# Kernel optimization log

Hardware: AMD Instinct MI355X
Metric: run time of the kernel (lower is better)

The kernel has to match this reference:

```python
import jax, jax.numpy as jnp
import numpy as np

V, D, H, B, S, T, N_EXTRA = 32000, 256, 512, 16, 400, 100, 50


def _lstm_cell(x, h, c, Wih, Whh, b):
    g = x @ Wih.T + h @ Whh.T + b
    i, f, gg, o = jnp.split(g, 4, axis=-1)
    c = jax.nn.sigmoid(f) * c + jax.nn.sigmoid(i) * jnp.tanh(gg)
    h = jax.nn.sigmoid(o) * jnp.tanh(c)
    return h, c


def _run_lstm(xs, m, Wih, Whh, b):
    # xs: [S,B,D], m: [S,B,1] validity mask (packed-sequence semantics)
    Bz, Hh = xs.shape[1], Whh.shape[1]
    init = (jnp.zeros((Bz, Hh), xs.dtype), jnp.zeros((Bz, Hh), xs.dtype))
    def step(carry, inp):
        h, c = carry
        x, mm = inp
        hn, cn = _lstm_cell(x, h, c, Wih, Whh, b)
        h = jnp.where(mm, hn, h)
        c = jnp.where(mm, cn, c)
        return (h, c), jnp.where(mm, hn, 0.0)
    (h, c), ys = jax.lax.scan(step, init, (xs, m))
    return ys, h, c


def setup_inputs():
    key = jax.random.key(0)
    ks = jax.random.split(key, 20)
    def gn(k, shape, scale=0.05):
        return jax.random.normal(k, shape, dtype=jnp.float32) * scale
    inp = {}
    inp["source"] = jax.random.randint(ks[0], (B, S), 0, V)
    inp["source_extended"] = jax.random.randint(ks[1], (B, S), 0, V + N_EXTRA)
    inp["source_length"] = jax.random.randint(ks[2], (B,), S // 2, S + 1)
    inp["target"] = jax.random.randint(ks[3], (B, T), 0, V)
    inp["emb"] = gn(ks[4], (V, D), 0.1)
    inp["enc_Wih_f"] = gn(ks[5], (4 * H, D))
    inp["enc_Whh_f"] = gn(ks[6], (4 * H, H))
    inp["enc_b_f"] = jnp.zeros((4 * H,), jnp.float32)
    inp["enc_Wih_b"] = gn(ks[7], (4 * H, D))
    inp["enc_Whh_b"] = gn(ks[8], (4 * H, H))
    inp["enc_b_b"] = jnp.zeros((4 * H,), jnp.float32)
    inp["Wproj"] = gn(ks[9], (H, 2 * H))
    inp["bproj"] = jnp.zeros((H,), jnp.float32)
    inp["W2h"] = gn(ks[10], (H, 2 * H))
    inp["b2h"] = jnp.zeros((H,), jnp.float32)
    inp["W2c"] = gn(ks[11], (H, 2 * H))
    inp["b2c"] = jnp.zeros((H,), jnp.float32)
    inp["Wo1"] = gn(ks[12], (H, 2 * H))
    inp["bo1"] = jnp.zeros((H,), jnp.float32)
    inp["Wo2"] = gn(ks[13], (D, H))
    inp["dec_Wih"] = gn(ks[14], (4 * H, 2 * D))
    inp["dec_Whh"] = gn(ks[15], (4 * H, H))
    inp["dec_b"] = jnp.zeros((4 * H,), jnp.float32)
    inp["Wpgen"] = gn(ks[16], (1, 2 * H + 2 * D))
    inp["bpgen"] = jnp.zeros((1,), jnp.float32)
    return inp


def reference(source, source_extended, source_length, target, emb,
              enc_Wih_f, enc_Whh_f, enc_b_f, enc_Wih_b, enc_Whh_b, enc_b_b,
              Wproj, bproj, W2h, b2h, W2c, b2c, Wo1, bo1, Wo2,
              dec_Wih, dec_Whh, dec_b, Wpgen, bpgen):
    mask = jnp.arange(S)[None, :] < source_length[:, None]  # [B,S]
    w_s = emb[source]                                        # [B,S,D]
    xs = jnp.swapaxes(w_s, 0, 1)                             # [S,B,D]
    m = jnp.swapaxes(mask, 0, 1)[:, :, None]                 # [S,B,1]
    # bidirectional LSTM encoder
    ys_f, h_f, c_f = _run_lstm(xs, m, enc_Wih_f, enc_Whh_f, enc_b_f)
    ys_b, h_b, c_b = _run_lstm(xs[::-1], m[::-1], enc_Wih_b, enc_Whh_b, enc_b_b)
    ys_b = ys_b[::-1]
    enc_outs = jnp.swapaxes(jnp.concatenate([ys_f, ys_b], -1), 0, 1)  # [B,S,2H]
    enc_outs = enc_outs @ Wproj.T + bproj                             # [B,S,H]
    dec_h = jnp.concatenate([h_f, h_b], -1) @ W2h.T + b2h             # [B,H]
    dec_c = jnp.concatenate([c_f, c_b], -1) @ W2c.T + b2c             # [B,H]
    lens = source_length[:, None].astype(enc_outs.dtype)
    seq_mean = (enc_outs * mask[..., None]).sum(1) / lens             # [B,H]
    def out_proj(x):
        return jnp.tanh(x @ Wo1.T + bo1) @ Wo2.T
    dec_out0 = out_proj(jnp.concatenate([dec_h, seq_mean], -1))       # [B,D]
    neg = jnp.finfo(enc_outs.dtype).min
    extra = jnp.zeros((B, N_EXTRA), enc_outs.dtype)
    rows = jnp.arange(B)[:, None]
    w_t = jnp.swapaxes(emb[target], 0, 1)                             # [T,B,D]
    def step(carry, x_t):
        dec_out, h, c = carry
        x = jnp.concatenate([x_t, dec_out], -1)                       # [B,2D]
        h, c = _lstm_cell(x, h, c, dec_Wih, dec_Whh, dec_b)
        scores = jnp.einsum('bh,bsh->bs', h, enc_outs)
        attn = jax.nn.softmax(jnp.where(mask, scores, neg), axis=-1)  # point_dist
        context = jnp.einsum('bs,bsh->bh', attn, enc_outs)
        p_gen = jax.nn.sigmoid(jnp.concatenate([context, h, x], -1) @ Wpgen.T + bpgen)  # [B,1]
        dec_out = out_proj(jnp.concatenate([h, context], -1))         # [B,D]
        logit = dec_out @ emb.T                                       # [B,V]
        vocab_dist = jnp.concatenate([p_gen * jax.nn.softmax(logit, axis=-1), extra], -1)
        final = vocab_dist.at[rows, source_extended].add((1.0 - p_gen) * attn) + 1e-20
        return (dec_out, h, c), jnp.log(final)
    _, logits = jax.lax.scan(step, (dec_out0, dec_h, dec_c), w_t)
    return logits  # [T,B,V+N_EXTRA]
```

## Files before the change

### kernel.cpp

```cpp
#include <hip/hip_runtime.h>

#define V_SZ 32000
#define D_SZ 256
#define H_SZ 512
#define B_SZ 16
#define S_SZ 400
#define T_SZ 100
#define G4   2048
#define VX   32050
#define LINE 32
#define SENTU 0xFFFFFFFFu

typedef unsigned short ushort_t;
typedef __attribute__((ext_vector_type(8))) __bf16 bf16x8;
typedef __attribute__((ext_vector_type(8))) unsigned short ushort8_t;
typedef __attribute__((ext_vector_type(4))) float f32x4;
typedef __attribute__((ext_vector_type(4))) unsigned u32x4;

__device__ __forceinline__ ushort_t f2bf(float x) {
  union { float f; unsigned u; } v; v.f = x;
  unsigned r = v.u + 0x7fffu + ((v.u >> 16) & 1u);
  return (ushort_t)(r >> 16);
}
__device__ __forceinline__ float bf2f(ushort_t x) {
  union { unsigned u; float f; } v; v.u = ((unsigned)x) << 16; return v.f;
}
__device__ __forceinline__ float bfu2f(unsigned x) {
  union { unsigned u; float f; } v; v.u = x << 16; return v.f;
}
__device__ __forceinline__ float sigf(float x) { return 1.0f / (1.0f + __expf(-x)); }
__device__ __forceinline__ float tanh_f(float x) {
  float e = __expf(2.0f * x);
  return 1.0f - 2.0f / (e + 1.0f);
}
__device__ __forceinline__ float dot4(f32x4 a, f32x4 b) {
  return a.x * b.x + a.y * b.y + a.z * b.z + a.w * b.w;
}
__device__ __forceinline__ void stg(float* p, float v) {
  __hip_atomic_store(p, v, __ATOMIC_RELAXED, __HIP_MEMORY_SCOPE_AGENT);
}
__device__ __forceinline__ void stg_u32(unsigned* p, unsigned v) {
  __hip_atomic_store(p, v, __ATOMIC_RELAXED, __HIP_MEMORY_SCOPE_AGENT);
}
__device__ __forceinline__ unsigned pollu(const unsigned* p) {
  return __hip_atomic_load(p, __ATOMIC_RELAXED, __HIP_MEMORY_SCOPE_AGENT);
}
__device__ __forceinline__ unsigned okq(u32x4 c) {
  return (unsigned)((c.x != SENTU) & (c.y != SENTU) & (c.z != SENTU) & (c.w != SENTU));
}
__device__ __forceinline__ u32x4 ld1_ic(const unsigned* p) {
  u32x4 v;
  asm volatile("global_load_dwordx4 %0, %1, off sc0 sc1\n\ts_waitcnt vmcnt(0)"
               : "=&v"(v) : "v"(p) : "memory");
  return v;
}

__device__ __forceinline__ void slot_barrier(unsigned* slots, int myslot, int nslots,
                                             unsigned pc) {
  asm volatile("s_waitcnt vmcnt(0)" ::: "memory");
  __syncthreads();
  if (threadIdx.x == 0)
    __hip_atomic_store(&slots[myslot * LINE], pc, __ATOMIC_RELAXED, __HIP_MEMORY_SCOPE_AGENT);
  if (threadIdx.x < 64) {
    const int i0 = threadIdx.x, i1 = threadIdx.x + 64, i2 = threadIdx.x + 128;
    for (;;) {
      unsigned v0 = pc, v1 = pc, v2 = pc;
      if (i0 < nslots) v0 = pollu(&slots[i0 * LINE]);
      if (i1 < nslots) v1 = pollu(&slots[i1 * LINE]);
      if (i2 < nslots) v2 = pollu(&slots[i2 * LINE]);
      if (__all((v0 >= pc) & (v1 >= pc) & (v2 >= pc))) break;
      __builtin_amdgcn_s_sleep(1);
    }
  }
  __syncthreads();
}

__global__ __launch_bounds__(256) void cvt_kernel(const float* in, ushort_t* outp, int n) {
  int i = blockIdx.x * 256 + threadIdx.x;
  int stride = gridDim.x * 256;
  for (; i < n; i += stride) outp[i] = f2bf(in[i]);
}

__global__ __launch_bounds__(256) void pack_whh_kernel(const float* whh_f, const float* whh_b,
                                                       ushort_t* outp) {
  int gid = blockIdx.x * 256 + threadIdx.x;
  int col = gid & 511;
  int p_g = gid >> 9;
  int dir = p_g >> 11, p = p_g & 2047;
  int ub = p >> 6, g = (p >> 4) & 3, u = p & 15;
  const float* src = dir ? whh_b : whh_f;
  outp[gid] = f2bf(src[(size_t)(g * 512 + ub * 16 + u) * 512 + col]);
}

__global__ __launch_bounds__(256) void gxT_kernel(const float* gx, float* gxT) {
  int t = blockIdx.y;
  int r = blockIdx.x * 256 + threadIdx.x;
  float v[16];
#pragma unroll
  for (int b = 0; b < 16; ++b) v[b] = gx[((size_t)t * 16 + b) * G4 + r];
  f32x4* dst = (f32x4*)(gxT + ((size_t)t * G4 + r) * 16);
#pragma unroll
  for (int q = 0; q < 4; ++q) {
    f32x4 w = {v[q * 4], v[q * 4 + 1], v[q * 4 + 2], v[q * 4 + 3]};
    dst[q] = w;
  }
}

__global__ __launch_bounds__(256) void gather_src_kernel(const ushort_t* emb_bf, const int* source,
                                                         ushort_t* xs_bf) {
  int gid = blockIdx.x * 256 + threadIdx.x;
  int r = gid >> 5, e = gid & 31;
  int s = r >> 4, b = r & 15;
  int tok = source[b * S_SZ + s];
  ((ushort8_t*)xs_bf)[gid] = ((const ushort8_t*)emb_bf)[(size_t)tok * 32 + e];
}

__device__ __forceinline__ void mfma_16x64(const ushort_t* A, const ushort_t* B_, int K,
                                           int m0, int n0, f32x4 acc[4]) {
  const int lane = threadIdx.x & 63;
  const int lr = lane & 15, kh = lane >> 4;
  const ushort_t* ap = A + (size_t)(m0 + lr) * K + kh * 8;
  const ushort_t* bp = B_ + (size_t)(n0 + lr) * K + kh * 8;
  for (int k0 = 0; k0 < K; k0 += 32) {
    bf16x8 av = *(const bf16x8*)(ap + k0);
#pragma unroll
    for (int s = 0; s < 4; ++s) {
      bf16x8 bv = *(const bf16x8*)(bp + (size_t)s * 16 * K + k0);
      acc[s] = __builtin_amdgcn_mfma_f32_16x16x32_bf16(av, bv, acc[s], 0, 0, 0);
    }
  }
}

__global__ __launch_bounds__(256) void gemm_abt_bias(const ushort_t* A, const ushort_t* Bm,
                                                     const float* bias, float* out, int K) {
  int wave = threadIdx.x >> 6;
  int m0 = blockIdx.y * 16;
  int n0 = blockIdx.x * 256 + wave * 64;
  f32x4 acc[4] = {};
  mfma_16x64(A, Bm, K, m0, n0, acc);
  int lane = threadIdx.x & 63, lr = lane & 15, kh = lane >> 4;
#pragma unroll
  for (int s = 0; s < 4; ++s) {
    int n = n0 + s * 16 + lr;
    float bv = bias[n];
#pragma unroll
    for (int i = 0; i < 4; ++i) {
      int m = m0 + kh * 4 + i;
      out[(size_t)m * G4 + n] = acc[s][i] + bv;
    }
  }
}

__global__ __launch_bounds__(256) void gemm_encout(const ushort_t* ys_cat, const ushort_t* wproj_bf,
                                                   const float* bproj, float* enc_outs) {
  int wave = threadIdx.x >> 6;
  int m0 = blockIdx.y * 16;
  int n0 = blockIdx.x * 256 + wave * 64;
  f32x4 acc[4] = {};
  mfma_16x64(ys_cat, wproj_bf, 2 * H_SZ, m0, n0, acc);
  int lane = threadIdx.x & 63, lr = lane & 15, kh = lane >> 4;
#pragma unroll
  for (int s = 0; s < 4; ++s) {
    int n = n0 + s * 16 + lr;
    float bv = bproj[n];
#pragma unroll
    for (int i = 0; i < 4; ++i) {
      int m = m0 + kh * 4 + i;
      int b = m & 15, si = m >> 4;
      enc_outs[((size_t)b * S_SZ + si) * H_SZ + n] = acc[s][i] + bv;
    }
  }
}

__global__ __launch_bounds__(256) void enc_kernel(
    const float* gx_f, const float* gx_b, const ushort_t* whh_pk, const int* src_len,
    unsigned* hbf_f, unsigned* hbf_b, unsigned* ys_cat_u32, float* h_final, float* c_final,
    unsigned* ctrs,
    const int* target, const ushort_t* emb_bf, ushort_t* xt_bf, const float* wo1,
    ushort_t* wo1_bf, const float* dwih, ushort_t* wihd_bf, const float* wo2,
    ushort_t* wo2t_bf, const float* wproj, ushort_t* wproj_bf, const float* wpgen, float* wfp,
    float* wfused, const float* dwhh, ushort_t* wdec_pk, ushort_t* e2_bf) {
  __shared__ float gates_s[4 * 16 * 17];
  __shared__ float xr_s[256];
  const int blk = blockIdx.x, tid = threadIdx.x;

  if (blk >= 64) {
    const int pid = blk - 64;
    const int gtid = pid * 256 + tid;
    const int GSTR = 192 * 256;
    for (int i = gtid; i < 512 * 1024; i += GSTR) wo1_bf[i] = f2bf(wo1[i]);
    for (int i = gtid; i < 2048 * 256; i += GSTR) {
      int r = i >> 8, d = i & 255;
      wihd_bf[i] = f2bf(dwih[(size_t)r * 512 + d]);
    }
    for (int i = gtid; i < 512 * 256; i += GSTR) {
      int h2 = i >> 8, d2 = i & 255;
      wo2t_bf[i] = f2bf(wo2[(size_t)d2 * 512 + h2]);
    }
    for (int i = gtid; i < 512 * 1024; i += GSTR) wproj_bf[i] = f2bf(wproj[i]);
    for (int i = gtid; i < 51200; i += GSTR) {
      int r = i >> 5, e = i & 31;
      int tt = r >> 4, bb = r & 15;
      int tok = target[bb * T_SZ + tt];
      ((ushort8_t*)xt_bf)[i] = ((const ushort8_t*)emb_bf)[(size_t)tok * 32 + e];
    }
    for (int h2 = gtid; h2 < 512; h2 += GSTR) {
      float a = 0;
      for (int d = 0; d < 256; ++d) a += wpgen[1280 + d] * wo2[(size_t)d * 512 + h2];
      wfp[h2] = a;
    }
    for (int r = pid; r < 2048; r += 192) {
      xr_s[tid] = dwih[(size_t)r * 512 + 256 + tid];
      __syncthreads();
      float a0 = 0, a1 = 0;
      for (int d = 0; d < 256; ++d) {
        float x = xr_s[d];
        a0 += x * wo2[(size_t)d * 512 + tid];
        a1 += x * wo2[(size_t)d * 512 + tid + 256];
      }
      wfused[(size_t)r * 512 + tid] = a0;
      wfused[(size_t)r * 512 + tid + 256] = a1;
      __syncthreads();
    }
    slot_barrier(ctrs + 2048, pid, 192, 1u);
    for (int i = gtid; i < 2048 * 1024; i += GSTR) {
      int col = i & 1023, p = i >> 10;
      int ub2 = p >> 4, g2 = (p >> 2) & 3, u2 = p & 3;
      int row = g2 * 512 + ub2 * 4 + u2;
      float v = (col < 512) ? dwhh[(size_t)row * 512 + col]
                            : wfused[(size_t)row * 512 + (col - 512)];
      wdec_pk[i] = f2bf(v);
    }
    for (int q = pid; q < 4000; q += 192) {
      int mt = q >> 1, xt2 = q & 1;
      int wave = tid >> 6;
      int m0 = mt * 16, n0 = xt2 * 256 + wave * 64;
      f32x4 acc[4] = {};
      mfma_16x64(emb_bf, wo2t_bf, 256, m0, n0, acc);
      int lane2 = tid & 63, lr2 = lane2 & 15, kh2 = lane2 >> 4;
#pragma unroll
      for (int s = 0; s < 4; ++s) {
        int n = n0 + s * 16 + lr2;
#pragma unroll
        for (int i = 0; i < 4; ++i) {
          int m = m0 + kh2 * 4 + i;
          e2_bf[(size_t)m * 512 + n] = f2bf(acc[s][i]);
        }
      }
    }
    return;
  }

  const int dir = blk >> 5, ub = blk & 31, j0 = ub * 16;
  const int g = tid >> 6, lane = tid & 63, lr = lane & 15, kh = lane >> 4;
  const float* gx = dir ? gx_b : gx_f;
  unsigned* hb = dir ? hbf_b : hbf_f;
  unsigned* slots = ctrs + dir * 1024;
  const ushort_t* wrow =
      whh_pk + (size_t)(((dir * 32 + ub) * 4 + g) * 16 + lr) * 512 + kh * 8;
  const int bc = tid >> 4, uc = tid & 15;
  const int len_b = src_len[bc];
  float c_reg = 0.0f, h_reg = 0.0f;

  int maxlen;
  {
    int v = src_len[lane & 15];
    v = max(v, __shfl_xor(v, 1));
    v = max(v, __shfl_xor(v, 2));
    v = max(v, __shfl_xor(v, 4));
    v = max(v, __shfl_xor(v, 8));
    maxlen = v;
  }
  for (int i = tid; i < (S_SZ - maxlen) * 128; i += 256) {
    int s = maxlen + (i >> 7);
    int r = i & 127;
    int bb = r >> 3, k = r & 7;
    ys_cat_u32[(size_t)(s * 16 + bb) * 512 + dir * 256 + (j0 >> 1) + k] = 0u;
  }

  float gxa[4];
  {
    const int s0 = dir ? (maxlen - 1) : 0;
    const float* g0 = gx + (size_t)s0 * (16 * 2048) + g * 512 + j0 + lr;
#pragma unroll
    for (int i = 0; i < 4; ++i) gxa[i] = g0[(size_t)(kh * 4 + i) * 2048];
  }

  for (int t = 0; t < maxlen; ++t) {
    const int s_pos = dir ? (maxlen - 1 - t) : t;
    float gxn[4] = {0.f, 0.f, 0.f, 0.f};
    if (t + 1 < maxlen) {
      const int sn = dir ? (maxlen - 2 - t) : (t + 1);
      const float* gn = gx + (size_t)sn * (16 * 2048) + g * 512 + j0 + lr;
#pragma unroll
      for (int i = 0; i < 4; ++i) gxn[i] = gn[(size_t)(kh * 4 + i) * 2048];
    }
    f32x4 acc = {0.f, 0.f, 0.f, 0.f};
    const ushort_t* ap = (const ushort_t*)(hb + (size_t)t * 4096) + lr * 512 + kh * 8;
#pragma unroll
    for (int k0 = 0; k0 < 512; k0 += 32)
      acc = __builtin_amdgcn_mfma_f32_16x16x32_bf16(*(const bf16x8*)(ap + k0),
                                                    *(const bf16x8*)(wrow + k0), acc, 0, 0, 0);
#pragma unroll
    for (int i = 0; i < 4; ++i)
      gates_s[(g * 16 + lr) * 17 + kh * 4 + i] = acc[i] + gxa[i];
    __syncthreads();
    float gi = gates_s[uc * 17 + bc];
    float gf = gates_s[(16 + uc) * 17 + bc];
    float gg = gates_s[(32 + uc) * 17 + bc];
    float go = gates_s[(48 + uc) * 17 + bc];
    bool msk = s_pos < len_b;
    float cn = sigf(gf) * c_reg + sigf(gi) * tanh_f(gg);
    float hn = sigf(go) * tanh_f(cn);
    float hout = msk ? hn : h_reg;
    if (msk) c_reg = cn;
    h_reg = hout;
    unsigned hbits = (unsigned)f2bf(hout);
    unsigned hpart = __shfl_xor(hbits, 1);
    unsigned ybits = msk ? (unsigned)f2bf(hn) : 0u;
    unsigned ypart = __shfl_xor(ybits, 1);
    if ((uc & 1) == 0) {
      stg_u32(&hb[(size_t)(t + 1) * 4096 + bc * 256 + ((j0 + uc) >> 1)], hbits | (hpart << 16));
      ys_cat_u32[(size_t)(s_pos * 16 + bc) * 512 + dir * 256 + ((j0 + uc) >> 1)] =
          ybits | (ypart << 16);
    }
    if (t == maxlen - 1) {
      h_final[dir * 8192 + bc * 512 + j0 + uc] = hout;
      c_final[dir * 8192 + bc * 512 + j0 + uc] = c_reg;
    }
    if (t + 1 < maxlen) slot_barrier(slots, ub, 32, (unsigned)(t + 1));
#pragma unroll
    for (int i = 0; i < 4; ++i) gxa[i] = gxn[i];
  }
}

__global__ __launch_bounds__(256) void seqmean_kernel(const float* enc_outs, const int* src_len,
                                                      float* seq_mean) {
  int b = blockIdx.x >> 1;
  int j = (blockIdx.x & 1) * 256 + threadIdx.x;
  int L = src_len[b];
  float a = 0;
  for (int s = 0; s < L; ++s) a += enc_outs[((size_t)b * S_SZ + s) * H_SZ + j];
  seq_mean[b * 512 + j] = a / (float)L;
}

__global__ __launch_bounds__(256) void init_state_kernel(const float* h_final, const float* c_final,
                                                         const float* w2h, const float* b2h,
                                                         const float* w2c, const float* b2c,
                                                         unsigned* h_u32, float* c_init) {
  int gid = blockIdx.x * 256 + threadIdx.x;
  int half = gid >> 13;
  int idx = gid & 8191;
  int b = idx >> 9, j = idx & 511;
  const float* src = half ? c_final : h_final;
  const float* w = (half ? w2c : w2h) + (size_t)j * 1024;
  float acc = (half ? b2c : b2h)[j];
  const f32x4* s0 = (const f32x4*)(src + b * 512);
  const f32x4* s1 = (const f32x4*)(src + 8192 + b * 512);
  const f32x4* w0 = (const f32x4*)w;
  const f32x4* w1 = w0 + 128;
  float a = 0;
  for (int k = 0; k < 128; ++k) a += dot4(s0[k], w0[k]);
  for (int k = 0; k < 128; ++k) a += dot4(s1[k], w1[k]);
  acc += a;
  if (half) {
    c_init[idx] = acc;
  } else {
    unsigned bits = (unsigned)f2bf(acc);
    unsigned pb2 = __shfl_xor(bits, 1);
    if ((j & 1) == 0) h_u32[b * 256 + (j >> 1)] = bits | (pb2 << 16);
  }
}

__global__ __launch_bounds__(256) void tmp0_kernel(const unsigned* h0_u32, const float* seq_mean,
                                                   const float* wo1, const float* bo1,
                                                   unsigned* tmp_u32) {
  int gid = blockIdx.x * 256 + threadIdx.x;
  int b = gid >> 9, j = gid & 511;
  const f32x4* x1 = (const f32x4*)(seq_mean + b * 512);
  const f32x4* w0 = (const f32x4*)(wo1 + (size_t)j * 1024);
  const f32x4* w1 = w0 + 128;
  float a = bo1[j];
  float p = 0;
  const ushort_t* h0 = (const ushort_t*)(h0_u32) + b * 512;
  for (int k = 0; k < 128; ++k) {
    f32x4 hv = {bf2f(h0[k * 4]), bf2f(h0[k * 4 + 1]), bf2f(h0[k * 4 + 2]), bf2f(h0[k * 4 + 3])};
    p += dot4(hv, w0[k]);
  }
  for (int k = 0; k < 128; ++k) p += dot4(x1[k], w1[k]);
  float tv = tanh_f(a + p);
  unsigned bits = (unsigned)f2bf(tv);
  unsigned pb2 = __shfl_xor(bits, 1);
  if ((j & 1) == 0) tmp_u32[b * 256 + (j >> 1)] = bits | (pb2 << 16);
}

__global__ __launch_bounds__(256) void dec_kernel(
    const ushort_t* xt_bf, const int* src_len, const ushort_t* wdec_pk,
    const float* wpgen, const float* bpgen, const float* wfp, const ushort_t* wo1_bf,
    const float* bo1, const float* enc_outs, const float* gxT, unsigned* h_u32,
    const float* c_init, unsigned* tmp_u32, float* ctx_part, float* z_part, float* zinv,
    float* pgen_o, float* pexp, unsigned* ctrs, const ushort_t* e2_bf, float* out) {
  __shared__ ushort_t ec_s[50 * 512];
  __shared__ float part_s[4 * 16 * 17];
  __shared__ f32x4 smem4[272];
  __shared__ float red_s[8];
  __shared__ float p_s[64];
  float* sm = (float*)smem4;
  unsigned* gslots = ctrs + 8192;

  const int blk = blockIdx.x, tid = threadIdx.x;

  if (blk >= 128) {
    const int sp = blk - 128;
    unsigned* tags = ctrs + 16384;
    if (sp == 0) {
      for (int t = 0; t < T_SZ; ++t) {
        if (tid < 64) {
          const unsigned* hp = tmp_u32 + (size_t)(t + 1) * 4096 + tid * 64;
          for (;;) {
            unsigned ok = 1;
#pragma unroll
            for (int k = 0; k < 16; ++k) ok &= okq(ld1_ic(hp + k * 4));
            if (__all((int)ok)) break;
            __builtin_amdgcn_s_sleep(8);
          }
          if (tid == 0) stg_u32(&tags[t * 32], 1u);
        }
        __syncthreads();
      }
    } else if (sp <= 125) {
      const ushort_t* tmp_bf2 = (const ushort_t*)(tmp_u32 + 4096);
      const int wave = tid >> 6;
      const int n0 = (sp - 1) * 256 + wave * 64;
      const int lane2 = tid & 63, lr2 = lane2 & 15, kh2 = lane2 >> 4;
      for (int t = 0; t < T_SZ; ++t) {
        if (tid < 64) {
          while (pollu(&tags[t * 32]) == 0u) __builtin_amdgcn_s_sleep(4);
        }
        __syncthreads();
        f32x4 acc[4] = {};
        mfma_16x64(tmp_bf2, e2_bf, 512, t * 16, n0, acc);
#pragma unroll
        for (int s = 0; s < 4; ++s) {
          int n = n0 + s * 16 + lr2;
#pragma unroll
          for (int i = 0; i < 4; ++i) {
            int m = t * 16 + kh2 * 4 + i;
            out[(size_t)m * VX + n] = acc[s][i];
          }
        }
      }
    }
    return;
  }

  const int w = tid >> 6, lane = tid & 63, lr = lane & 15, kh = lane >> 4;
  const int j0 = blk * 4;
  const ushort_t* wrow = wdec_pk + (size_t)(blk * 16 + lr) * 1024 + w * 256 + kh * 8;
  const int b_c = (tid >> 2) & 15, u_c = tid & 3;
  float c_reg = (tid < 64) ? c_init[b_c * 512 + j0 + u_c] : 0.0f;
  const int b_pb = blk >> 3, ch = blk & 7, s0c = ch * 50;
  const int len_pb = src_len[b_pb];
  const int nc = ch;
  unsigned* grslots = ctrs + 12288 + b_pb * 256;
  unsigned gpc = 0;

  {
    const f32x4* ebase = (const f32x4*)(enc_outs + ((size_t)b_pb * S_SZ + s0c) * H_SZ);
    unsigned* dst = (unsigned*)ec_s;
    for (int i = tid; i < 6400; i += 256) {
      f32x4 v = ebase[i];
      dst[2 * i] = (unsigned)f2bf(v.x) | ((unsigned)f2bf(v.y) << 16);
      dst[2 * i + 1] = (unsigned)f2bf(v.z) | ((unsigned)f2bf(v.w) << 16);
    }
  }

  float gxa[4] = {0.f, 0.f, 0.f, 0.f};
  if (tid < 64) {
#pragma unroll
    for (int g2 = 0; g2 < 4; ++g2)
      gxa[g2] = gxT[((size_t)(g2 * 512 + j0 + u_c)) * 16 + b_c];
  }

  for (int t = 0; t < T_SZ; ++t) {
    {
      f32x4 acc = {0.f, 0.f, 0.f, 0.f};
      const unsigned* asrc = (w < 2) ? (h_u32 + (size_t)t * 4096) : (tmp_u32 + (size_t)t * 4096);
      const ushort_t* ap = (const ushort_t*)asrc + lr * 512 + (w & 1) * 256 + kh * 8;
#pragma unroll
      for (int k0 = 0; k0 < 256; k0 += 32)
        acc = __builtin_amdgcn_mfma_f32_16x16x32_bf16(*(const bf16x8*)(ap + k0),
                                                      *(const bf16x8*)(wrow + k0), acc, 0, 0, 0);
#pragma unroll
      for (int i = 0; i < 4; ++i) part_s[(w * 16 + lr) * 17 + kh * 4 + i] = acc[i];
      __syncthreads();
      if (tid < 64) {
        float gt[4];
#pragma unroll
        for (int g2 = 0; g2 < 4; ++g2) {
          int p = g2 * 4 + u_c;
          float a = gxa[g2];
#pragma unroll
          for (int w2 = 0; w2 < 4; ++w2) a += part_s[(w2 * 16 + p) * 17 + b_c];
          gt[g2] = a;
        }
        float cn = sigf(gt[1]) * c_reg + sigf(gt[0]) * tanh_f(gt[2]);
        c_reg = cn;
        float hn = sigf(gt[3]) * tanh_f(cn);
        unsigned bits = (unsigned)f2bf(hn);
        unsigned pb2 = __shfl_xor(bits, 1);
        if ((u_c & 1) == 0)
          stg_u32(&h_u32[(size_t)(t + 1) * 4096 + b_c * 256 + ((j0 + u_c) >> 1)],
                  bits | (pb2 << 16));
      }
    }
    slot_barrier(gslots, blk, 128, ++gpc);
    {
      if (tid < 64 && t + 1 < T_SZ) {
#pragma unroll
        for (int g2 = 0; g2 < 4; ++g2)
          gxa[g2] = gxT[((size_t)(t + 1) * G4 + g2 * 512 + j0 + u_c) * 16 + b_c];
      }
      if (tid < 128) {
        unsigned v0 = h_u32[(size_t)(t + 1) * 4096 + b_pb * 256 + tid * 2];
        unsigned v1 = h_u32[(size_t)(t + 1) * 4096 + b_pb * 256 + tid * 2 + 1];
        f32x4 hv = {bfu2f(v0 & 0xffffu), bfu2f(v0 >> 16), bfu2f(v1 & 0xffffu), bfu2f(v1 >> 16)};
        ((f32x4*)sm)[tid] = hv;
      }
      __syncthreads();
      int st = tid >> 2, kq = tid & 3;
      if (st < 50) {
        const ushort8_t* er = (const ushort8_t*)(ec_s + st * 512) + kq * 16;
        const f32x4* hr = (const f32x4*)sm + kq * 32;
        float sc = 0;
#pragma unroll 4
        for (int k = 0; k < 16; ++k) {
          ushort8_t w8 = er[k];
          f32x4 w0 = {bf2f(w8[0]), bf2f(w8[1]), bf2f(w8[2]), bf2f(w8[3])};
          f32x4 w1 = {bf2f(w8[4]), bf2f(w8[5]), bf2f(w8[6]), bf2f(w8[7])};
          sc += dot4(hr[2 * k], w0) + dot4(hr[2 * k + 1], w1);
        }
        sc += __shfl_xor(sc, 1);
        sc += __shfl_xor(sc, 2);
        if (kq == 0) {
          int s_abs = s0c + st;
          float p = (s_abs < len_pb) ? __expf(sc) : 0.0f;
          p_s[st] = p;
          pexp[((size_t)t * 16 + b_pb) * S_SZ + s_abs] = p;
        }
      }
      __syncthreads();
      if (tid == 0) {
        float z = 0;
        for (int s = 0; s < 50; ++s) z += p_s[s];
        stg(&z_part[((size_t)t * 16 + b_pb) * 8 + ch], z);
      }
      float a0 = 0, a1 = 0;
      for (int s = 0; s < 50; ++s) {
        float p = p_s[s];
        a0 += p * bf2f(ec_s[s * 512 + tid]);
        a1 += p * bf2f(ec_s[s * 512 + tid + 256]);
      }
      float* cp = ctx_part + (((size_t)t * 16 + b_pb) * 8 + ch) * 512;
      stg(&cp[tid], a0);
      stg(&cp[tid + 256], a1);
    }
    slot_barrier(grslots, ch, 8, (unsigned)(t + 1));
    {
      float* h_s = sm;
      float* ctx_s = sm + 512;
      const float* zp = z_part + ((size_t)t * 16 + b_pb) * 8;
      float z = 0;
#pragma unroll
      for (int c2 = 0; c2 < 8; ++c2) z += zp[c2];
      float inv = 1.0f / z;
      const float* cpb = ctx_part + ((size_t)t * 16 + b_pb) * 8 * 512;
      float c0 = 0, c1 = 0;
#pragma unroll
      for (int c2 = 0; c2 < 8; ++c2) {
        c0 += cpb[c2 * 512 + tid];
        c1 += cpb[c2 * 512 + tid + 256];
      }
      ctx_s[tid] = c0 * inv;
      ctx_s[tid + 256] = c1 * inv;
      __syncthreads();
      const ushort_t* tmpp = (const ushort_t*)(tmp_u32 + (size_t)t * 4096) + b_pb * 512;
      float tp0 = bf2f(tmpp[tid]);
      float tp1 = bf2f(tmpp[tid + 256]);
      float xe = bf2f(xt_bf[((size_t)t * 16 + b_pb) * 256 + tid]);
      float pg = wpgen[tid] * ctx_s[tid] + wpgen[tid + 256] * ctx_s[tid + 256] +
                 wpgen[512 + tid] * h_s[tid] + wpgen[512 + tid + 256] * h_s[tid + 256] +
                 wpgen[1024 + tid] * xe + wfp[tid] * tp0 + wfp[tid + 256] * tp1;
#pragma unroll
      for (int o = 32; o; o >>= 1) pg += __shfl_xor(pg, o);
      if (lane == 0) red_s[w] = pg;
      __syncthreads();
      if (nc == 0 && tid == 0) {
        pgen_o[t * 16 + b_pb] = sigf(red_s[0] + red_s[1] + red_s[2] + red_s[3] + bpgen[0]);
        zinv[t * 16 + b_pb] = inv;
      }
      int nidx = tid >> 2, kq = tid & 3;
      int n = nc * 64 + nidx;
      const ushort8_t* wrp = (const ushort8_t*)(wo1_bf + (size_t)n * 1024) + kq * 32;
      const f32x4* xr2 =
          (kq < 2) ? ((const f32x4*)h_s + kq * 64) : ((const f32x4*)ctx_s + (kq - 2) * 64);
      float a = 0;
#pragma unroll 4
      for (int k = 0; k < 32; ++k) {
        ushort8_t w8 = wrp[k];
        f32x4 w0 = {bf2f(w8[0]), bf2f(w8[1]), bf2f(w8[2]), bf2f(w8[3])};
        f32x4 w1 = {bf2f(w8[4]), bf2f(w8[5]), bf2f(w8[6]), bf2f(w8[7])};
        a += dot4(xr2[2 * k], w0) + dot4(xr2[2 * k + 1], w1);
      }
      a += __shfl_xor(a, 1);
      a += __shfl_xor(a, 2);
      float tv = tanh_f(a + bo1[n]);
      unsigned bits = (unsigned)f2bf(tv);
      unsigned pbits = __shfl_xor(bits, 4);
      if (kq == 0 && (nidx & 1) == 0)
        stg_u32(&tmp_u32[(size_t)(t + 1) * 4096 + b_pb * 256 + ((nc * 64 + nidx) >> 1)],
                bits | (pbits << 16));
    }
    if (t + 1 < T_SZ) slot_barrier(gslots, blk, 128, ++gpc);
  }
}

__global__ __launch_bounds__(1024) void finalize_kernel(float* out, const float* pexp,
                                                        const float* zinv, const float* pgen_i,
                                                        const int* src_ext) {
  __shared__ float scat[VX];
  __shared__ float red[64];
  const int row = blockIdx.x;
  const int b = row & 15;
  const int tid = threadIdx.x;
  for (int i = tid; i < VX; i += 1024) scat[i] = 0.0f;
  __syncthreads();
  const float pg = pgen_i[row];
  const float inv = zinv[row];
  if (tid < S_SZ) {
    float v = (1.0f - pg) * pexp[(size_t)row * S_SZ + tid] * inv;
    int col = src_ext[b * S_SZ + tid];
    atomicAdd(&scat[col], v);
  }
  float* orow = out + (size_t)row * VX;
  float l[32];
  float mx = -3.4e38f;
#pragma unroll
  for (int i2 = 0; i2 < 32; ++i2) {
    int col = tid + (i2 << 10);
    l[i2] = (col < V_SZ) ? orow[col] : -3.4e38f;
    mx = fmaxf(mx, l[i2]);
  }
#pragma unroll
  for (int o = 32; o; o >>= 1) mx = fmaxf(mx, __shfl_xor(mx, o));
  if ((tid & 63) == 0) red[16 + (tid >> 6)] = mx;
  __syncthreads();
  if (tid == 0) {
    float m2 = red[16];
    for (int w = 1; w < 16; ++w) m2 = fmaxf(m2, red[16 + w]);
    red[0] = m2;
  }
  __syncthreads();
  const float gmx = red[0];
  float se = 0.0f;
#pragma unroll
  for (int i2 = 0; i2 < 32; ++i2) {
    int col = tid + (i2 << 10);
    if (col < V_SZ) {
      l[i2] = __expf(l[i2] - gmx);
      se += l[i2];
    }
  }
#pragma unroll
  for (int o = 32; o; o >>= 1) se += __shfl_xor(se, o);
  if ((tid & 63) == 0) red[32 + (tid >> 6)] = se;
  __syncthreads();
  if (tid == 0) {
    float s2 = 0;
    for (int w = 0; w < 16; ++w) s2 += red[32 + w];
    red[1] = s2;
  }
  __syncthreads();
  const float scale = pg / red[1];
#pragma unroll
  for (int i2 = 0; i2 < 32; ++i2) {
    int col = tid + (i2 << 10);
    if (col < VX) {
      float base = (col < V_SZ) ? l[i2] * scale : 0.0f;
      orow[col] = __logf(base + scat[col] + 1e-20f);
    }
  }
}

extern "C" void kernel_launch(void* const* d_in, const int* in_sizes, int n_in, void* d_out,
                              int out_size, void* d_ws, size_t ws_size, hipStream_t stream) {
  (void)in_sizes; (void)n_in; (void)out_size; (void)ws_size;
  const int* source = (const int*)d_in[0];
  const int* source_ext = (const int*)d_in[1];
  const int* source_len = (const int*)d_in[2];
  const int* target = (const int*)d_in[3];
  const float* emb = (const float*)d_in[4];
  const float* wih_f = (const float*)d_in[5];
  const float* whh_f = (const float*)d_in[6];
  const float* b_f = (const float*)d_in[7];
  const float* wih_b = (const float*)d_in[8];
  const float* whh_b = (const float*)d_in[9];
  const float* b_b = (const float*)d_in[10];
  const float* wproj = (const float*)d_in[11];
  const float* bproj = (const float*)d_in[12];
  const float* w2h = (const float*)d_in[13];
  const float* b2h = (const float*)d_in[14];
  const float* w2c = (const float*)d_in[15];
  const float* b2c = (const float*)d_in[16];
  const float* wo1 = (const float*)d_in[17];
  const float* bo1 = (const float*)d_in[18];
  const float* wo2 = (const float*)d_in[19];
  const float* dwih = (const float*)d_in[20];
  const float* dwhh = (const float*)d_in[21];
  const float* dbias = (const float*)d_in[22];
  const float* wpgen = (const float*)d_in[23];
  const float* bpgen = (const float*)d_in[24];
  float* out = (float*)d_out;

  size_t off = 0;
  char* wsb = (char*)d_ws;
  auto alloc = [&](size_t bytes) -> void* {
    void* p = wsb + off;
    off += (bytes + 255) & ~(size_t)255;
    return p;
  };
  unsigned* ctrs = (unsigned*)alloc(80 * 1024);
  ushort_t* emb_bf = (ushort_t*)alloc((size_t)V_SZ * D_SZ * 2);
  ushort_t* wihf_bf = (ushort_t*)alloc((size_t)G4 * D_SZ * 2);
  ushort_t* wihb_bf = (ushort_t*)alloc((size_t)G4 * D_SZ * 2);
  ushort_t* wihd_bf = (ushort_t*)alloc((size_t)G4 * D_SZ * 2);
  ushort_t* wproj_bf = (ushort_t*)alloc((size_t)H_SZ * 2 * H_SZ * 2);
  ushort_t* wo2t_bf = (ushort_t*)alloc((size_t)H_SZ * D_SZ * 2);
  ushort_t* wo1_bf = (ushort_t*)alloc((size_t)H_SZ * 1024 * 2);
  float* wfused = (float*)alloc((size_t)G4 * H_SZ * 4);
  float* wfp = (float*)alloc(512 * 4);
  ushort_t* whh_pk = (ushort_t*)alloc((size_t)2 * G4 * H_SZ * 2);
  ushort_t* wdec_pk = (ushort_t*)alloc((size_t)G4 * 1024 * 2);
  ushort_t* xs_bf = (ushort_t*)alloc((size_t)S_SZ * B_SZ * D_SZ * 2);
  ushort_t* xt_bf = (ushort_t*)alloc((size_t)T_SZ * B_SZ * D_SZ * 2);
  ushort_t* e2_bf = (ushort_t*)alloc((size_t)V_SZ * H_SZ * 2);
  float* gx_f = (float*)alloc((size_t)S_SZ * B_SZ * G4 * 4);
  float* gx_b = (float*)alloc((size_t)S_SZ * B_SZ * G4 * 4);
  unsigned* hbf_f = (unsigned*)alloc((size_t)(S_SZ + 1) * 4096 * 4);
  unsigned* hbf_b = (unsigned*)alloc((size_t)(S_SZ + 1) * 4096 * 4);
  unsigned* ys_cat_u32 = (unsigned*)alloc((size_t)S_SZ * B_SZ * 512 * 4);
  float* h_final = (float*)alloc((size_t)2 * B_SZ * H_SZ * 4);
  float* c_final = (float*)alloc((size_t)2 * B_SZ * H_SZ * 4);
  float* enc_outs = (float*)alloc((size_t)B_SZ * S_SZ * H_SZ * 4);
  float* seq_mean = (float*)alloc((size_t)B_SZ * H_SZ * 4);
  unsigned* h_u32 = (unsigned*)alloc((size_t)(T_SZ + 1) * 4096 * 4);
  float* c_init = (float*)alloc((size_t)B_SZ * H_SZ * 4);
  unsigned* tmp_u32 = (unsigned*)alloc((size_t)(T_SZ + 1) * 4096 * 4);
  float* z_part = (float*)alloc((size_t)T_SZ * B_SZ * 8 * 4);
  float* zinv = (float*)alloc((size_t)T_SZ * B_SZ * 4);
  float* pgen_b = (float*)alloc((size_t)T_SZ * B_SZ * 4);
  float* pexp = (float*)alloc((size_t)T_SZ * B_SZ * S_SZ * 4);
  float* gx_dec = gx_b;
  float* ctx_part = gx_b + (size_t)3276800;
  float* gxT = gx_b + (size_t)9830400;

  hipMemsetAsync(ctrs, 0, 80 * 1024, stream);
  hipMemsetAsync(tmp_u32, 0xFF, (size_t)(T_SZ + 1) * 4096 * 4, stream);
  hipMemsetAsync(hbf_f, 0, 4096 * 4, stream);
  hipMemsetAsync(hbf_b, 0, 4096 * 4, stream);

  cvt_kernel<<<2048, 256, 0, stream>>>(emb, emb_bf, V_SZ * D_SZ);
  cvt_kernel<<<2048, 256, 0, stream>>>(wih_f, wihf_bf, G4 * D_SZ);
  cvt_kernel<<<2048, 256, 0, stream>>>(wih_b, wihb_bf, G4 * D_SZ);
  pack_whh_kernel<<<8192, 256, 0, stream>>>(whh_f, whh_b, whh_pk);
  gather_src_kernel<<<800, 256, 0, stream>>>(emb_bf, source, xs_bf);
  gemm_abt_bias<<<dim3(8, 400), 256, 0, stream>>>(xs_bf, wihf_bf, b_f, gx_f, 256);
  gemm_abt_bias<<<dim3(8, 400), 256, 0, stream>>>(xs_bf, wihb_bf, b_b, gx_b, 256);
  enc_kernel<<<256, 256, 0, stream>>>(gx_f, gx_b, whh_pk, source_len, hbf_f, hbf_b, ys_cat_u32,
                                      h_final, c_final, ctrs, target, emb_bf, xt_bf, wo1, wo1_bf,
                                      dwih, wihd_bf, wo2, wo2t_bf, wproj, wproj_bf, wpgen, wfp,
                                      wfused, dwhh, wdec_pk, e2_bf);
  gemm_encout<<<dim3(2, 400), 256, 0, stream>>>((const ushort_t*)ys_cat_u32, wproj_bf, bproj,
                                                enc_outs);
  seqmean_kernel<<<32, 256, 0, stream>>>(enc_outs, source_len, seq_mean);
  init_state_kernel<<<64, 256, 0, stream>>>(h_final, c_final, w2h, b2h, w2c, b2c, h_u32, c_init);
  tmp0_kernel<<<32, 256, 0, stream>>>(h_u32, seq_mean, wo1, bo1, tmp_u32);
  gemm_abt_bias<<<dim3(8, 100), 256, 0, stream>>>(xt_bf, wihd_bf, dbias, gx_dec, 256);
  gxT_kernel<<<dim3(8, 100), 256, 0, stream>>>(gx_dec, gxT);
  dec_kernel<<<256, 256, 0, stream>>>(xt_bf, source_len, wdec_pk, wpgen, bpgen, wfp, wo1_bf, bo1,
                                      enc_outs, gxT, h_u32, c_init, tmp_u32, ctx_part, z_part,
                                      zinv, pgen_b, pexp, ctrs, e2_bf, out);
  finalize_kernel<<<1600, 1024, 0, stream>>>(out, pexp, zinv, pgen_b, source_ext);
}
```

Baseline: 4.317 ms.

## Merge prologue conversions, batch gate GEMMs, fold decoder input GEMM into encoder helpers

The separate conversion, packing and gather kernels are merged into a single prologue kernel. The two encoder input-gate GEMMs become one launch via a z-dimension. The decoder input-projection GEMM and its transpose now run inside the encoder kernel's idle helper blocks, writing directly in the transposed gxT layout. The aim is to cut launch count and move decoder prep off the critical path. In exchange it adds work to the helper blocks, which must finish before the encoder kernel exits, and it relies on xt_bf and wihd_bf being written earlier in the same helper block.

After: 4.281 ms. About the same (-0.8%).

```diff
diff --git a/kernel.cpp b/kernel.cpp
--- a/kernel.cpp
+++ b/kernel.cpp
@@ -75,44 +75,31 @@
   __syncthreads();
 }
 
-__global__ __launch_bounds__(256) void cvt_kernel(const float* in, ushort_t* outp, int n) {
-  int i = blockIdx.x * 256 + threadIdx.x;
-  int stride = gridDim.x * 256;
-  for (; i < n; i += stride) outp[i] = f2bf(in[i]);
-}
-
-__global__ __launch_bounds__(256) void pack_whh_kernel(const float* whh_f, const float* whh_b,
-                                                       ushort_t* outp) {
-  int gid = blockIdx.x * 256 + threadIdx.x;
-  int col = gid & 511;
-  int p_g = gid >> 9;
-  int dir = p_g >> 11, p = p_g & 2047;
-  int ub = p >> 6, g = (p >> 4) & 3, u = p & 15;
-  const float* src = dir ? whh_b : whh_f;
-  outp[gid] = f2bf(src[(size_t)(g * 512 + ub * 16 + u) * 512 + col]);
-}
-
-__global__ __launch_bounds__(256) void gxT_kernel(const float* gx, float* gxT) {
-  int t = blockIdx.y;
-  int r = blockIdx.x * 256 + threadIdx.x;
-  float v[16];
-#pragma unroll
-  for (int b = 0; b < 16; ++b) v[b] = gx[((size_t)t * 16 + b) * G4 + r];
-  f32x4* dst = (f32x4*)(gxT + ((size_t)t * G4 + r) * 16);
-#pragma unroll
-  for (int q = 0; q < 4; ++q) {
-    f32x4 w = {v[q * 4], v[q * 4 + 1], v[q * 4 + 2], v[q * 4 + 3]};
-    dst[q] = w;
-  }
-}
-
-__global__ __launch_bounds__(256) void gather_src_kernel(const ushort_t* emb_bf, const int* source,
-                                                         ushort_t* xs_bf) {
-  int gid = blockIdx.x * 256 + threadIdx.x;
-  int r = gid >> 5, e = gid & 31;
-  int s = r >> 4, b = r & 15;
-  int tok = source[b * S_SZ + s];
-  ((ushort8_t*)xs_bf)[gid] = ((const ushort8_t*)emb_bf)[(size_t)tok * 32 + e];
+__global__ __launch_bounds__(256) void prologue_kernel(const float* emb, const float* wih_f,
+                                                       const float* wih_b, const float* whh_f,
+                                                       const float* whh_b, const int* source,
+                                                       ushort_t* emb_bf, ushort_t* wihf_bf,
+                                                       ushort_t* wihb_bf, ushort_t* whh_pk,
+                                                       ushort_t* xs_bf) {
+  const int gtid = blockIdx.x * 256 + threadIdx.x;
+  const int GSTR = 2048 * 256;
+  for (int i = gtid; i < V_SZ * D_SZ; i += GSTR) emb_bf[i] = f2bf(emb[i]);
+  for (int i = gtid; i < G4 * D_SZ; i += GSTR) wihf_bf[i] = f2bf(wih_f[i]);
+  for (int i = gtid; i < G4 * D_SZ; i += GSTR) wihb_bf[i] = f2bf(wih_b[i]);
+  for (int i = gtid; i < 2 * G4 * H_SZ; i += GSTR) {
+    int col = i & 511;
+    int p_g = i >> 9;
+    int dir = p_g >> 11, p = p_g & 2047;
+    int ub = p >> 6, g = (p >> 4) & 3, u = p & 15;
+    const float* src = dir ? whh_b : whh_f;
+    whh_pk[i] = f2bf(src[(size_t)(g * 512 + ub * 16 + u) * 512 + col]);
+  }
+  for (int i = gtid; i < S_SZ * B_SZ * D_SZ; i += GSTR) {
+    int row = i >> 8, d = i & 255;
+    int s = row >> 4, b = row & 15;
+    int tok = source[b * S_SZ + s];
+    xs_bf[i] = f2bf(emb[(size_t)tok * 256 + d]);
+  }
 }
 
 __device__ __forceinline__ void mfma_16x64(const ushort_t* A, const ushort_t* B_, int K,
@@ -131,13 +118,18 @@
   }
 }
 
-__global__ __launch_bounds__(256) void gemm_abt_bias(const ushort_t* A, const ushort_t* Bm,
-                                                     const float* bias, float* out, int K) {
+__global__ __launch_bounds__(256) void gemm_gates2(const ushort_t* A, const ushort_t* Bf,
+                                                   const ushort_t* Bb, const float* bias_f,
+                                                   const float* bias_b, float* out_f,
+                                                   float* out_b) {
   int wave = threadIdx.x >> 6;
   int m0 = blockIdx.y * 16;
   int n0 = blockIdx.x * 256 + wave * 64;
+  const ushort_t* Bm = blockIdx.z ? Bb : Bf;
+  const float* bias = blockIdx.z ? bias_b : bias_f;
+  float* out = blockIdx.z ? out_b : out_f;
   f32x4 acc[4] = {};
-  mfma_16x64(A, Bm, K, m0, n0, acc);
+  mfma_16x64(A, Bm, D_SZ, m0, n0, acc);
   int lane = threadIdx.x & 63, lr = lane & 15, kh = lane >> 4;
 #pragma unroll
   for (int s = 0; s < 4; ++s) {
@@ -179,7 +171,8 @@
     const int* target, const ushort_t* emb_bf, ushort_t* xt_bf, const float* wo1,
     ushort_t* wo1_bf, const float* dwih, ushort_t* wihd_bf, const float* wo2,
     ushort_t* wo2t_bf, const float* wproj, ushort_t* wproj_bf, const float* wpgen, float* wfp,
-    float* wfused, const float* dwhh, ushort_t* wdec_pk, ushort_t* e2_bf) {
+    float* wfused, const float* dwhh, ushort_t* wdec_pk, ushort_t* e2_bf, const float* dbias,
+    float* gxT) {
   __shared__ float gates_s[4 * 16 * 17];
   __shared__ float xr_s[256];
   const int blk = blockIdx.x, tid = threadIdx.x;
@@ -245,6 +238,24 @@
         for (int i = 0; i < 4; ++i) {
           int m = m0 + kh2 * 4 + i;
           e2_bf[(size_t)m * 512 + n] = f2bf(acc[s][i]);
+        }
+      }
+    }
+    for (int q = pid; q < 800; q += 192) {
+      int mt = q >> 3, nt = q & 7;
+      int wave = tid >> 6;
+      int m0 = mt * 16, n0 = nt * 256 + wave * 64;
+      f32x4 acc[4] = {};
+      mfma_16x64(xt_bf, wihd_bf, 256, m0, n0, acc);
+      int lane2 = tid & 63, lr2 = lane2 & 15, kh2 = lane2 >> 4;
+#pragma unroll
+      for (int s = 0; s < 4; ++s) {
+        int n = n0 + s * 16 + lr2;
+        float bv = dbias[n];
+#pragma unroll
+        for (int i = 0; i < 4; ++i) {
+          int b = kh2 * 4 + i;
+          gxT[((size_t)mt * G4 + n) * 16 + b] = acc[s][i] + bv;
         }
       }
     }
@@ -744,6 +755,7 @@
   ushort_t* xs_bf = (ushort_t*)alloc((size_t)S_SZ * B_SZ * D_SZ * 2);
   ushort_t* xt_bf = (ushort_t*)alloc((size_t)T_SZ * B_SZ * D_SZ * 2);
   ushort_t* e2_bf = (ushort_t*)alloc((size_t)V_SZ * H_SZ * 2);
+  float* gxT = (float*)alloc((size_t)T_SZ * B_SZ * G4 * 4);
   float* gx_f = (float*)alloc((size_t)S_SZ * B_SZ * G4 * 4);
   float* gx_b = (float*)alloc((size_t)S_SZ * B_SZ * G4 * 4);
   unsigned* hbf_f = (unsigned*)alloc((size_t)(S_SZ + 1) * 4096 * 4);
@@ -760,33 +772,25 @@
   float* zinv = (float*)alloc((size_t)T_SZ * B_SZ * 4);
   float* pgen_b = (float*)alloc((size_t)T_SZ * B_SZ * 4);
   float* pexp = (float*)alloc((size_t)T_SZ * B_SZ * S_SZ * 4);
-  float* gx_dec = gx_b;
   float* ctx_part = gx_b + (size_t)3276800;
-  float* gxT = gx_b + (size_t)9830400;
 
   hipMemsetAsync(ctrs, 0, 80 * 1024, stream);
   hipMemsetAsync(tmp_u32, 0xFF, (size_t)(T_SZ + 1) * 4096 * 4, stream);
   hipMemsetAsync(hbf_f, 0, 4096 * 4, stream);
   hipMemsetAsync(hbf_b, 0, 4096 * 4, stream);
 
-  cvt_kernel<<<2048, 256, 0, stream>>>(emb, emb_bf, V_SZ * D_SZ);
-  cvt_kernel<<<2048, 256, 0, stream>>>(wih_f, wihf_bf, G4 * D_SZ);
-  cvt_kernel<<<2048, 256, 0, stream>>>(wih_b, wihb_bf, G4 * D_SZ);
-  pack_whh_kernel<<<8192, 256, 0, stream>>>(whh_f, whh_b, whh_pk);
-  gather_src_kernel<<<800, 256, 0, stream>>>(emb_bf, source, xs_bf);
-  gemm_abt_bias<<<dim3(8, 400), 256, 0, stream>>>(xs_bf, wihf_bf, b_f, gx_f, 256);
-  gemm_abt_bias<<<dim3(8, 400), 256, 0, stream>>>(xs_bf, wihb_bf, b_b, gx_b, 256);
+  prologue_kernel<<<2048, 256, 0, stream>>>(emb, wih_f, wih_b, whh_f, whh_b, source, emb_bf,
+                                            wihf_bf, wihb_bf, whh_pk, xs_bf);
+  gemm_gates2<<<dim3(8, 400, 2), 256, 0, stream>>>(xs_bf, wihf_bf, wihb_bf, b_f, b_b, gx_f, gx_b);
   enc_kernel<<<256, 256, 0, stream>>>(gx_f, gx_b, whh_pk, source_len, hbf_f, hbf_b, ys_cat_u32,
                                       h_final, c_final, ctrs, target, emb_bf, xt_bf, wo1, wo1_bf,
                                       dwih, wihd_bf, wo2, wo2t_bf, wproj, wproj_bf, wpgen, wfp,
-                                      wfused, dwhh, wdec_pk, e2_bf);
+                                      wfused, dwhh, wdec_pk, e2_bf, dbias, gxT);
   gemm_encout<<<dim3(2, 400), 256, 0, stream>>>((const ushort_t*)ys_cat_u32, wproj_bf, bproj,
                                                 enc_outs);
   seqmean_kernel<<<32, 256, 0, stream>>>(enc_outs, source_len, seq_mean);
   init_state_kernel<<<64, 256, 0, stream>>>(h_final, c_final, w2h, b2h, w2c, b2c, h_u32, c_init);
   tmp0_kernel<<<32, 256, 0, stream>>>(h_u32, seq_mean, wo1, bo1, tmp_u32);
-  gemm_abt_bias<<<dim3(8, 100), 256, 0, stream>>>(xt_bf, wihd_bf, dbias, gx_dec, 256);
-  gxT_kernel<<<dim3(8, 100), 256, 0, stream>>>(gx_dec, gxT);
   dec_kernel<<<256, 256, 0, stream>>>(xt_bf, source_len, wdec_pk, wpgen, bpgen, wfp, wo1_bf, bo1,
                                       enc_outs, gxT, h_u32, c_init, tmp_u32, ctx_part, z_part,
                                       zinv, pgen_b, pexp, ctrs, e2_bf, out);
```
